# Performance work log

Hardware: AMD Instinct MI355X
Metric: run time of the kernel (lower is better)

Reference implementation:

```python
import jax, jax.numpy as jnp
import numpy as np

N, E, D_IN, HID, HEADS, TS_OUT = 100000, 200000, 165, 64, 8, 5
HD1 = HID // HEADS  # 8 per-head channels in layer 1
HD2 = HID           # 64 per-head channels in layer 2 (concat=False -> mean)


def _glorot(key, shape):
    fan_in, fan_out = shape[0], shape[1]
    s = np.sqrt(6.0 / (fan_in + fan_out)).astype(np.float32)
    return jax.random.uniform(key, shape, jnp.float32, -s, s)


def setup_inputs() -> dict:
    key = jax.random.key(0)
    ks = jax.random.split(key, 24)
    inp = {
        "x": jax.random.normal(ks[0], (N, D_IN), jnp.float32),
        "edge_index": jax.random.randint(ks[1], (2, E), 0, N, jnp.int32),
        "timestamp_target": jax.random.randint(ks[2], (N,), 0, TS_OUT, jnp.int32),
        "node_target": jax.random.randint(ks[3], (N,), 0, 2, jnp.int32),
        "node_mask": jax.random.randint(ks[4], (N,), 0, 2, jnp.int32).astype(jnp.bool_),
        # GATConv layer 1: in=165 -> 8 heads x 8 ch, concat -> 64
        "W1": _glorot(ks[5], (D_IN, HEADS * HD1)),
        "att_src1": _glorot(ks[6], (HEADS, HD1)),
        "att_dst1": _glorot(ks[7], (HEADS, HD1)),
        "b1": jnp.zeros((HEADS * HD1,), jnp.float32),
        # GATConv layer 2: in=64 -> 8 heads x 64 ch, mean -> 64
        "W2": _glorot(ks[8], (HID, HEADS * HD2)),
        "att_src2": _glorot(ks[9], (HEADS, HD2)),
        "att_dst2": _glorot(ks[10], (HEADS, HD2)),
        "b2": jnp.zeros((HD2,), jnp.float32),
        # timestamp predictor MLP
        "ts_w1": _glorot(ks[11], (HID, HID)), "ts_b1": jnp.zeros((HID,), jnp.float32),
        "ts_w2": _glorot(ks[12], (HID, TS_OUT)), "ts_b2": jnp.zeros((TS_OUT,), jnp.float32),
        # class predictor MLP
        "cls_w1": _glorot(ks[13], (HID, HID)), "cls_b1": jnp.zeros((HID,), jnp.float32),
        "cls_w2": _glorot(ks[14], (HID, 2)), "cls_b2": jnp.zeros((2,), jnp.float32),
    }
    return inp


def _gat_layer(x, src, dst, n, W, a_src, a_dst, b, concat):
    H, C = a_src.shape
    h = (x @ W).reshape(n, H, C)                      # [N,H,C]
    a_s = (h * a_src).sum(-1)                         # [N,H]
    a_d = (h * a_dst).sum(-1)                         # [N,H]
    alpha = jax.nn.leaky_relu(a_s[src] + a_d[dst], 0.2)   # [E,H]
    amax = jax.ops.segment_max(alpha, dst, num_segments=n)
    ea = jnp.exp(alpha - amax[dst])
    denom = jax.ops.segment_sum(ea, dst, num_segments=n)
    a = ea / (denom[dst] + 1e-16)                     # segment softmax over incoming edges
    out = jax.ops.segment_sum(h[src] * a[:, :, None], dst, num_segments=n)  # [N,H,C]
    out = out.reshape(n, H * C) if concat else out.mean(axis=1)
    return out + b


def _ce(logits, targets):
    lp = jax.nn.log_softmax(logits, axis=-1)
    return -jnp.take_along_axis(lp, targets[:, None].astype(jnp.int32), axis=1)[:, 0]


def reference(x, edge_index, timestamp_target, node_target, node_mask,
              W1, att_src1, att_dst1, b1, W2, att_src2, att_dst2, b2,
              ts_w1, ts_b1, ts_w2, ts_b2, cls_w1, cls_b1, cls_w2, cls_b2):
    n = x.shape[0]
    loops = jnp.arange(n, dtype=edge_index.dtype)
    src = jnp.concatenate([edge_index[0], loops])     # add self loops (PyG default)
    dst = jnp.concatenate([edge_index[1], loops])
    h = _gat_layer(x, src, dst, n, W1, att_src1, att_dst1, b1, True)   # [N,64]
    h = _gat_layer(h, src, dst, n, W2, att_src2, att_dst2, b2, False)  # [N,64]
    # gradient reversal is identity in the forward pass
    ts_pred = jax.nn.relu(h @ ts_w1 + ts_b1) @ ts_w2 + ts_b2           # [N,5]
    cls_pred = jax.nn.relu(h @ cls_w1 + cls_b1) @ cls_w2 + cls_b2      # [N,2]
    ts_loss = _ce(ts_pred, timestamp_target).mean()
    m = node_mask.astype(jnp.float32)
    cls_loss = (_ce(cls_pred, node_target) * m).sum() / m.sum()
    return cls_loss + 1.0 * ts_loss
```

## Files before the change

### kernel.cpp

```cpp
#include <hip/hip_runtime.h>
#include <hip/hip_bf16.h>

#define NN 100000
#define NE 200000
#define NT (NE + NN)
#define DIN 165
#define PREPB 128
#define INITB 391
#define PACKB 32
#define W1PB 24
#define MISCGRID (PREPB + INITB + PACKB + W1PB)
#define NODEB 1563
#define XDW ((size_t)NN * DIN)
#define G1ROWS 32
#define G1NDMA 21

typedef __attribute__((ext_vector_type(8))) short bf16x8_t;
typedef __attribute__((ext_vector_type(4))) float f32x4_t;
typedef _Float16 h2_t __attribute__((ext_vector_type(2)));
typedef _Float16 f16x8_t __attribute__((ext_vector_type(8)));

#define AS1 __attribute__((address_space(1)))
#define AS3 __attribute__((address_space(3)))

static __device__ __forceinline__ unsigned short f2bf(float f) {
    __hip_bfloat16 b = __float2bfloat16(f);
    return *(unsigned short*)&b;
}
static __device__ __forceinline__ float bfu(unsigned short u) {
    __hip_bfloat16 b = *(__hip_bfloat16*)&u;
    return __bfloat162float(b);
}
static __device__ __forceinline__ unsigned pkh2(float a, float b) {
    h2_t v; v[0] = (_Float16)a; v[1] = (_Float16)b;
    return *(unsigned*)&v;
}


__global__ __launch_bounds__(256) void k_misc(const float* W2, const float* a2s, const float* a2d,
                                              float* wsd, __hip_bfloat16* W2pT,
                                              int* cnt, int* fill,
                                              const float* tsw1, const float* cw1,
                                              __hip_bfloat16* wB,
                                              const float* W1, unsigned* W1pT, float* zbuf) {
    int b = blockIdx.x;
    int tid = threadIdx.x;
    if (b < PREPB) {
        int i = b * 256 + tid;
        int c = i >> 9, j = i & 511;
        int hh = j >> 6, kk = j & 63;
        W2pT[i] = __float2bfloat16(W2[kk * 512 + hh * 64 + c]);
        if (b == 0) zbuf[tid] = 0.f;
        if (i < 512) {
            int h = i >> 6, k = i & 63;
            float s = 0.f, d = 0.f;
            for (int cc = 0; cc < 64; cc++) {
                float w = W2[k * 512 + h * 64 + cc];
                s += w * a2s[h * 64 + cc];
                d += w * a2d[h * 64 + cc];
            }
            wsd[i] = s; wsd[512 + i] = d;
        }
    } else if (b < PREPB + INITB) {
        int i = (b - PREPB) * 256 + tid;
        if (i < NN) { cnt[i] = 0; fill[i] = 0; }
    } else if (b < PREPB + INITB + PACKB) {
        int i = (b - PREPB - INITB) * 256 + tid;
        if (i < 8192) {
            int c = i >> 6, k = i & 63;
            float v = (c < 64) ? tsw1[k * 64 + c] : cw1[k * 64 + (c - 64)];
            wB[i] = __float2bfloat16(v);
        }
    } else {
        int i = (b - PREPB - INITB - PACKB) * 256 + tid;
        if (i < 6144) {
            int c = i / 96, kp = i - c * 96;
            int k = 2 * kp;
            float f0 = (k < DIN) ? W1[k * 64 + c] : 0.f;
            float f1 = (k + 1 < DIN) ? W1[(k + 1) * 64 + c] : 0.f;
            W1pT[i] = pkh2(f0, f1);
        }
    }
}


__global__ __launch_bounds__(256) void k_count(const int* dstE, int* cnt) {
    int e = blockIdx.x * 256 + threadIdx.x;
    if (e < NE) atomicAdd(&cnt[dstE[e]], 1);
}

__global__ __launch_bounds__(256) void k_scanA(const int* cnt, int* rowptr, int* bsum) {
    __shared__ int sm[256];
    int t = threadIdx.x;
    int base = blockIdx.x * 1024;
    int v[4]; int s = 0;
    for (int i = 0; i < 4; i++) {
        int idx = base + t * 4 + i;
        v[i] = (idx < NN) ? (cnt[idx] + 1) : 0;
        s += v[i];
    }
    sm[t] = s; __syncthreads();
    for (int off = 1; off < 256; off <<= 1) {
        int x = (t >= off) ? sm[t - off] : 0;
        __syncthreads();
        sm[t] += x;
        __syncthreads();
    }
    int run = sm[t] - s;
    for (int i = 0; i < 4; i++) {
        run += v[i];
        int idx = base + t * 4 + i;
        if (idx < NN) rowptr[idx + 1] = run;
    }
    if (t == 255) bsum[blockIdx.x] = sm[255];
}

__global__ __launch_bounds__(64) void k_scanB(int* bsum, int nb) {
    int lane = threadIdx.x;
    int v0 = (lane < nb) ? bsum[lane] : 0;
    int v1 = (64 + lane < nb) ? bsum[64 + lane] : 0;
    int s0 = v0;
    for (int off = 1; off < 64; off <<= 1) { int t = __shfl_up(s0, off); if (lane >= off) s0 += t; }
    int tot0 = __shfl(s0, 63);
    int s1 = v1;
    for (int off = 1; off < 64; off <<= 1) { int t = __shfl_up(s1, off); if (lane >= off) s1 += t; }
    if (lane < nb) bsum[lane] = s0 - v0;
    if (64 + lane < nb) bsum[64 + lane] = tot0 + s1 - v1;
}

__global__ __launch_bounds__(256) void k_scanC(const int* bsum, int* rowptr) {
    int i = blockIdx.x * 256 + threadIdx.x;
    if (i < NN) rowptr[i + 1] += bsum[i >> 10];
    if (i == 0) rowptr[0] = 0;
}

__global__ __launch_bounds__(256) void k_fill(const int* srcE, const int* dstE,
                                              const int* rowptr, int* fill, int* col, int* rowv) {
    int i = blockIdx.x * 256 + threadIdx.x;
    if (i >= NT) return;
    int s, d;
    if (i < NE) { s = srcE[i]; d = dstE[i]; }
    else        { s = i - NE; d = s; }
    int p = rowptr[d] + atomicAdd(&fill[d], 1);
    col[p] = s;
    rowv[p] = d;
}


__global__ __launch_bounds__(128) void k_gemm1(const float* x, const unsigned* W1pT,
                                               const float* att_s, const float* att_d,
                                               const float* zsrc,
                                               __hip_bfloat16* h1b, float* aad1) {
    __shared__ float X[G1NDMA * 256];
    int tid = threadIdx.x;
    int l = tid & 63, w = tid >> 6;
    int n0 = blockIdx.x * G1ROWS;
    int frow = l & 15, kg = l >> 4;

    size_t tb = (size_t)n0 * DIN;
    for (int i = w; i < G1NDMA; i += 2) {
        size_t gd = tb + (size_t)i * 256 + (size_t)l * 4;
        const float* g = (gd + 4 <= XDW) ? (x + gd) : (zsrc + l * 4);
        __builtin_amdgcn_global_load_lds((const AS1 float*)g,
                                         (AS3 float*)(X + i * 256), 16, 0, 0);
    }
    uint4 B[6][4];
    #pragma unroll
    for (int s = 0; s < 6; s++)
        #pragma unroll
        for (int t = 0; t < 4; t++)
            B[s][t] = *(const uint4*)&W1pT[(t * 16 + frow) * 96 + s * 16 + kg * 4];
    __syncthreads();

    f32x4_t acc[4] = {};
    int rbase = (w * 16 + frow) * DIN + kg * 8;
    #pragma unroll
    for (int s = 0; s < 6; s++) {
        f16x8_t av;
        #pragma unroll
        for (int j = 0; j < 8; j++) av[j] = (_Float16)X[rbase + s * 32 + j];
        #pragma unroll
        for (int t = 0; t < 4; t++)
            acc[t] = __builtin_amdgcn_mfma_f32_16x16x32_f16(av, *(f16x8_t*)&B[s][t], acc[t], 0, 0, 0);
    }

    int nw = n0 + w * 16;
    float asv[4], adv[4];
    #pragma unroll
    for (int t = 0; t < 4; t++) {
        int c = t * 16 + frow;
        asv[t] = att_s[c]; adv[t] = att_d[c];
    }
    int hb = (l >> 3) & 1;
    #pragma unroll
    for (int q = 0; q < 4; q++) {
        int n = nw + kg * 4 + q;
        #pragma unroll
        for (int t = 0; t < 4; t++) {
            float sv = acc[t][q] * asv[t];
            float dv = acc[t][q] * adv[t];
            sv += __shfl_xor(sv, 1); sv += __shfl_xor(sv, 2); sv += __shfl_xor(sv, 4);
            dv += __shfl_xor(dv, 1); dv += __shfl_xor(dv, 2); dv += __shfl_xor(dv, 4);
            if ((l & 7) == 0) {
                int h = t * 2 + hb;
                aad1[(size_t)n * 16 + h]     = sv;
                aad1[(size_t)n * 16 + 8 + h] = dv;
            }
        }
    }

    __syncthreads();
    unsigned short* Hw = (unsigned short*)X + w * 1152;
    #pragma unroll
    for (int t = 0; t < 4; t++)
        #pragma unroll
        for (int q = 0; q < 4; q++)
            Hw[(kg * 4 + q) * 72 + t * 16 + frow] = f2bf(acc[t][q]);
    int rr = l >> 2, cc = l & 3;
    int n2 = nw + rr;
    unsigned short* dst = (unsigned short*)h1b + (size_t)n2 * 64 + cc * 16;
    *(uint4*)dst       = *(const uint4*)&Hw[rr * 72 + cc * 16];
    *(uint4*)(dst + 8) = *(const uint4*)&Hw[rr * 72 + cc * 16 + 8];
}


__global__ __launch_bounds__(256) void k_edgew(const float* aad, const int* col, const int* rowv,
                                               __hip_bfloat16* web) {
    int e = blockIdx.x * 256 + threadIdx.x;
    if (e >= NT) return;
    int s = col[e], d = rowv[e];
    float4 s0 = *(const float4*)&aad[(size_t)s * 16];
    float4 s1 = *(const float4*)&aad[(size_t)s * 16 + 4];
    float4 dd0 = *(const float4*)&aad[(size_t)d * 16 + 8];
    float4 dd1 = *(const float4*)&aad[(size_t)d * 16 + 12];
    float as[8] = {s0.x, s0.y, s0.z, s0.w, s1.x, s1.y, s1.z, s1.w};
    float ad[8] = {dd0.x, dd0.y, dd0.z, dd0.w, dd1.x, dd1.y, dd1.z, dd1.w};
    unsigned p[4];
    #pragma unroll
    for (int q = 0; q < 4; q++) {
        float a0 = as[2*q]   + ad[2*q];
        float a1 = as[2*q+1] + ad[2*q+1];
        a0 = a0 > 0.f ? a0 : 0.2f * a0;
        a1 = a1 > 0.f ? a1 : 0.2f * a1;
        p[q] = (unsigned)f2bf(__expf(a0)) | ((unsigned)f2bf(__expf(a1)) << 16);
    }
    *(uint4*)&web[(size_t)e * 8] = make_uint4(p[0], p[1], p[2], p[3]);
}


__global__ __launch_bounds__(256) void k_agg1(const __hip_bfloat16* h1b, const __hip_bfloat16* we1b,
                                              const int* rowptr, const int* col,
                                              const float* b1, __hip_bfloat16* out1b) {
    int tid = threadIdx.x;
    int q = tid & 15;
    int n = blockIdx.x * 16 + (tid >> 4);
    int hq = q >> 1;
    const unsigned short* h1u = (const unsigned short*)h1b;
    const unsigned short* weu = (const unsigned short*)we1b;
    int rs = rowptr[n], re = rowptr[n + 1];
    float acc0 = 0.f, acc1 = 0.f, acc2 = 0.f, acc3 = 0.f, den = 0.f;
    for (int eb = rs; eb < re; eb += 4) {
        int c4[4];
        #pragma unroll
        for (int j = 0; j < 4; j++) c4[j] = col[min(eb + j, re - 1)];
        #pragma unroll
        for (int j = 0; j < 4; j++) {
            int e = min(eb + j, re - 1);
            float wv = bfu(weu[(size_t)e * 8 + hq]);
            wv = (eb + j < re) ? wv : 0.f;
            uint2 hv = *(const uint2*)&h1u[(size_t)c4[j] * 64 + q * 4];
            den  += wv;
            acc0 += wv * bfu((unsigned short)(hv.x & 0xffff));
            acc1 += wv * bfu((unsigned short)(hv.x >> 16));
            acc2 += wv * bfu((unsigned short)(hv.y & 0xffff));
            acc3 += wv * bfu((unsigned short)(hv.y >> 16));
        }
    }
    float4 bb = *(const float4*)&b1[q * 4];
    float dd = den + 1e-16f;
    unsigned short* ou = (unsigned short*)out1b;
    unsigned p0 = (unsigned)f2bf(acc0 / dd + bb.x) | ((unsigned)f2bf(acc1 / dd + bb.y) << 16);
    unsigned p1 = (unsigned)f2bf(acc2 / dd + bb.z) | ((unsigned)f2bf(acc3 / dd + bb.w) << 16);
    *(uint2*)&ou[(size_t)n * 64 + q * 4] = make_uint2(p0, p1);
}


__global__ __launch_bounds__(256) void k_att2(const __hip_bfloat16* out1b, const float* wsd,
                                              float* aad2) {
    __shared__ float t[64][65];
    int tid = threadIdx.x;
    int n0 = blockIdx.x * 64;
    const unsigned short* o1u = (const unsigned short*)out1b;
    #pragma unroll
    for (int l = 0; l < 4; l++) {
        int q = tid + l * 256;
        int r = q >> 4, c4 = q & 15;
        int n = n0 + r;
        uint2 v = make_uint2(0, 0);
        if (n < NN) v = *(const uint2*)&o1u[(size_t)n * 64 + c4 * 4];
        t[r][c4 * 4 + 0] = bfu((unsigned short)(v.x & 0xffff));
        t[r][c4 * 4 + 1] = bfu((unsigned short)(v.x >> 16));
        t[r][c4 * 4 + 2] = bfu((unsigned short)(v.y & 0xffff));
        t[r][c4 * 4 + 3] = bfu((unsigned short)(v.y >> 16));
    }
    __syncthreads();
    int lane = tid & 63;
    int j0 = __builtin_amdgcn_readfirstlane((tid >> 6) * 4);
    int n = n0 + lane;
    float a0 = 0.f, a1 = 0.f, a2 = 0.f, a3 = 0.f;
    #pragma unroll 8
    for (int k = 0; k < 64; k++) {
        float ov = t[lane][k];
        a0 += ov * wsd[(j0 + 0) * 64 + k];
        a1 += ov * wsd[(j0 + 1) * 64 + k];
        a2 += ov * wsd[(j0 + 2) * 64 + k];
        a3 += ov * wsd[(j0 + 3) * 64 + k];
    }
    if (n < NN) *(float4*)&aad2[(size_t)n * 16 + j0] = make_float4(a0, a1, a2, a3);
}


__global__ __launch_bounds__(256) void k_l2f(const __hip_bfloat16* out1b, const __hip_bfloat16* we2b,
                                             const int* rowptr, const int* col,
                                             const __hip_bfloat16* W2pT, const float* b2,
                                             const __hip_bfloat16* wB,
                                             const float* tsb1, const float* cb1,
                                             const float* tsw2, const float* tsb2,
                                             const float* cw2, const float* cb2,
                                             const int* tst, const int* ctg, const unsigned char* msk,
                                             float* part) {
    __shared__ unsigned short Ax[64 * 512];
    __shared__ unsigned short Bl[64 * 72];
    __shared__ float red[4][3];
    int tid = threadIdx.x;
    int l = tid & 63, w = tid >> 6;
    int n0 = blockIdx.x * 64;
    int frow = l & 15, kg = l >> 4;

    const unsigned short* o1u = (const unsigned short*)out1b;
    const unsigned short* weu = (const unsigned short*)we2b;
    int q4 = tid & 15;
    #pragma unroll 1
    for (int pass = 0; pass < 4; pass++) {
        int j = pass * 16 + (tid >> 4);
        int n = n0 + j;
        int rs = 0, re = 0;
        if (n < NN) { rs = rowptr[n]; re = rowptr[n + 1]; }
        float acc[8][4];
        float den[8];
        #pragma unroll
        for (int h = 0; h < 8; h++) {
            den[h] = 0.f;
            #pragma unroll
            for (int c = 0; c < 4; c++) acc[h][c] = 0.f;
        }
        for (int eb = rs; eb < re; eb += 4) {
            int c4[4];
            #pragma unroll
            for (int jj = 0; jj < 4; jj++) c4[jj] = col[min(eb + jj, re - 1)];
            #pragma unroll
            for (int jj = 0; jj < 4; jj++) {
                int e = min(eb + jj, re - 1);
                uint4 wv = *(const uint4*)&weu[(size_t)e * 8];
                uint2 hv = *(const uint2*)&o1u[(size_t)c4[jj] * 64 + q4 * 4];
                float vm = (eb + jj < re) ? 1.f : 0.f;
                float hc0 = bfu((unsigned short)(hv.x & 0xffff));
                float hc1 = bfu((unsigned short)(hv.x >> 16));
                float hc2 = bfu((unsigned short)(hv.y & 0xffff));
                float hc3 = bfu((unsigned short)(hv.y >> 16));
                float wt[8] = {bfu((unsigned short)(wv.x & 0xffff)), bfu((unsigned short)(wv.x >> 16)),
                               bfu((unsigned short)(wv.y & 0xffff)), bfu((unsigned short)(wv.y >> 16)),
                               bfu((unsigned short)(wv.z & 0xffff)), bfu((unsigned short)(wv.z >> 16)),
                               bfu((unsigned short)(wv.w & 0xffff)), bfu((unsigned short)(wv.w >> 16))};
                #pragma unroll
                for (int h = 0; h < 8; h++) {
                    float ww = wt[h] * vm;
                    den[h] += ww;
                    acc[h][0] += ww * hc0;
                    acc[h][1] += ww * hc1;
                    acc[h][2] += ww * hc2;
                    acc[h][3] += ww * hc3;
                }
            }
        }
        #pragma unroll
        for (int h = 0; h < 8; h++) {
            float dd = den[h] + 1e-16f;
            unsigned lo = (unsigned)f2bf(acc[h][0] / dd) | ((unsigned)f2bf(acc[h][1] / dd) << 16);
            unsigned hi = (unsigned)f2bf(acc[h][2] / dd) | ((unsigned)f2bf(acc[h][3] / dd) << 16);
            int blk = (h * 8 + (q4 >> 1)) ^ (j & 7);
            *(uint2*)&Ax[j * 512 + blk * 8 + (q4 & 1) * 4] = make_uint2(lo, hi);
        }
    }
    __syncthreads();

    const unsigned short* B_g = (const unsigned short*)W2pT;
    f32x4_t gacc[4] = {};
    for (int k0 = 0; k0 < 512; k0 += 64) {
        #pragma unroll
        for (int ll = 0; ll < 2; ll++) {
            int u = tid + ll * 256;
            int r = u >> 3, seg = u & 7;
            *(uint4*)&Bl[r * 72 + seg * 8] = *(const uint4*)&B_g[(size_t)r * 512 + k0 + seg * 8];
        }
        __syncthreads();
        #pragma unroll
        for (int kk = 0; kk < 2; kk++) {
            int blk = ((k0 >> 3) + kk * 4 + kg) ^ (frow & 7);
            bf16x8_t a = *(const bf16x8_t*)&Ax[(w * 16 + frow) * 512 + blk * 8];
            #pragma unroll
            for (int t = 0; t < 4; t++) {
                bf16x8_t bb = *(const bf16x8_t*)&Bl[(t * 16 + frow) * 72 + kk * 32 + kg * 8];
                gacc[t] = __builtin_amdgcn_mfma_f32_16x16x32_bf16(a, bb, gacc[t], 0, 0, 0);
            }
        }
        __syncthreads();
    }

    unsigned short* o2L = Ax;
    #pragma unroll
    for (int t = 0; t < 4; t++) {
        float bias = b2[t * 16 + frow];
        #pragma unroll
        for (int q = 0; q < 4; q++)
            o2L[(w * 16 + kg * 4 + q) * 72 + t * 16 + frow] = f2bf(0.125f * gacc[t][q] + bias);
    }
    __syncthreads();
    const unsigned short* wBu = (const unsigned short*)wB;
    f32x4_t a2c[8] = {};
    #pragma unroll
    for (int kk = 0; kk < 2; kk++) {
        bf16x8_t a2 = *(const bf16x8_t*)&o2L[(w * 16 + frow) * 72 + kk * 32 + kg * 8];
        #pragma unroll
        for (int t2 = 0; t2 < 8; t2++) {
            bf16x8_t b2f = *(const bf16x8_t*)&wBu[(t2 * 16 + frow) * 64 + kk * 32 + kg * 8];
            a2c[t2] = __builtin_amdgcn_mfma_f32_16x16x32_bf16(a2, b2f, a2c[t2], 0, 0, 0);
        }
    }

    float lg[4][5]; float lc[4][2];
    #pragma unroll
    for (int q = 0; q < 4; q++) {
        #pragma unroll
        for (int t = 0; t < 5; t++) lg[q][t] = 0.f;
        lc[q][0] = 0.f; lc[q][1] = 0.f;
    }
    #pragma unroll
    for (int t2 = 0; t2 < 4; t2++) {
        int c = t2 * 16 + frow;
        float bb = tsb1[c];
        float w0 = tsw2[c * 5 + 0], w1 = tsw2[c * 5 + 1], w2 = tsw2[c * 5 + 2],
              w3 = tsw2[c * 5 + 3], w4 = tsw2[c * 5 + 4];
        #pragma unroll
        for (int q = 0; q < 4; q++) {
            float v = fmaxf(a2c[t2][q] + bb, 0.f);
            lg[q][0] += v * w0; lg[q][1] += v * w1; lg[q][2] += v * w2;
            lg[q][3] += v * w3; lg[q][4] += v * w4;
        }
    }
    #pragma unroll
    for (int t2 = 0; t2 < 4; t2++) {
        int c = t2 * 16 + frow;
        float bb = cb1[c];
        float u0 = cw2[c * 2], u1 = cw2[c * 2 + 1];
        #pragma unroll
        for (int q = 0; q < 4; q++) {
            float v = fmaxf(a2c[t2 + 4][q] + bb, 0.f);
            lc[q][0] += v * u0; lc[q][1] += v * u1;
        }
    }
    #pragma unroll
    for (int q = 0; q < 4; q++) {
        #pragma unroll
        for (int t = 0; t < 5; t++) {
            lg[q][t] += __shfl_xor(lg[q][t], 1);
            lg[q][t] += __shfl_xor(lg[q][t], 2);
            lg[q][t] += __shfl_xor(lg[q][t], 4);
            lg[q][t] += __shfl_xor(lg[q][t], 8);
        }
        #pragma unroll
        for (int t = 0; t < 2; t++) {
            lc[q][t] += __shfl_xor(lc[q][t], 1);
            lc[q][t] += __shfl_xor(lc[q][t], 2);
            lc[q][t] += __shfl_xor(lc[q][t], 4);
            lc[q][t] += __shfl_xor(lc[q][t], 8);
        }
    }
    float tsl = 0.f, cll = 0.f, mval = 0.f;
    if (frow == 0) {
        #pragma unroll
        for (int q = 0; q < 4; q++) {
            int n = n0 + w * 16 + kg * 4 + q;
            if (n < NN) {
                float L[5];
                #pragma unroll
                for (int t = 0; t < 5; t++) L[t] = lg[q][t] + tsb2[t];
                float mx = fmaxf(fmaxf(fmaxf(L[0], L[1]), fmaxf(L[2], L[3])), L[4]);
                float se = 0.f;
                #pragma unroll
                for (int t = 0; t < 5; t++) se += __expf(L[t] - mx);
                int tg = tst[n];
                float pick = 0.f;
                #pragma unroll
                for (int t = 0; t < 5; t++) pick += (t == tg) ? L[t] : 0.f;
                tsl += mx + __logf(se) - pick;
                float C0 = lc[q][0] + cb2[0];
                float C1 = lc[q][1] + cb2[1];
                float mx2 = fmaxf(C0, C1);
                float lse2 = mx2 + __logf(__expf(C0 - mx2) + __expf(C1 - mx2));
                float mv = msk[n] ? 1.f : 0.f;
                float pick2 = ctg[n] ? C1 : C0;
                cll += (lse2 - pick2) * mv;
                mval += mv;
            }
        }
    }
    #pragma unroll
    for (int off = 1; off < 64; off <<= 1) {
        tsl  += __shfl_xor(tsl, off);
        cll  += __shfl_xor(cll, off);
        mval += __shfl_xor(mval, off);
    }
    if (l == 0) { red[w][0] = tsl; red[w][1] = cll; red[w][2] = mval; }
    __syncthreads();
    if (tid == 0) {
        part[blockIdx.x * 3 + 0] = red[0][0] + red[1][0] + red[2][0] + red[3][0];
        part[blockIdx.x * 3 + 1] = red[0][1] + red[1][1] + red[2][1] + red[3][1];
        part[blockIdx.x * 3 + 2] = red[0][2] + red[1][2] + red[2][2] + red[3][2];
    }
}

__global__ __launch_bounds__(256) void k_final(const float* part, float* out, int nb) {
    __shared__ float sm[3][256];
    int tid = threadIdx.x;
    float a = 0, b = 0, c = 0;
    for (int i = tid; i < nb; i += 256) { a += part[i*3]; b += part[i*3+1]; c += part[i*3+2]; }
    sm[0][tid] = a; sm[1][tid] = b; sm[2][tid] = c;
    __syncthreads();
    for (int s = 128; s > 0; s >>= 1) {
        if (tid < s) {
            sm[0][tid] += sm[0][tid + s];
            sm[1][tid] += sm[1][tid + s];
            sm[2][tid] += sm[2][tid + s];
        }
        __syncthreads();
    }
    if (tid == 0) out[0] = sm[1][0] / sm[2][0] + sm[0][0] / (float)NN;
}


extern "C" void kernel_launch(void* const* d_in, const int* in_sizes, int n_in,
                              void* d_out, int out_size, void* d_ws, size_t ws_size,
                              hipStream_t stream) {
    const float* x    = (const float*)d_in[0];
    const int*   ei   = (const int*)d_in[1];
    const int*   tst  = (const int*)d_in[2];
    const int*   ctg  = (const int*)d_in[3];
    const unsigned char* msk = (const unsigned char*)d_in[4];
    const float* W1   = (const float*)d_in[5];
    const float* a1s  = (const float*)d_in[6];
    const float* a1d  = (const float*)d_in[7];
    const float* b1   = (const float*)d_in[8];
    const float* W2   = (const float*)d_in[9];
    const float* a2s  = (const float*)d_in[10];
    const float* a2d  = (const float*)d_in[11];
    const float* b2   = (const float*)d_in[12];
    const float* tsw1 = (const float*)d_in[13];
    const float* tsb1 = (const float*)d_in[14];
    const float* tsw2 = (const float*)d_in[15];
    const float* tsb2 = (const float*)d_in[16];
    const float* cw1  = (const float*)d_in[17];
    const float* cb1  = (const float*)d_in[18];
    const float* cw2  = (const float*)d_in[19];
    const float* cb2  = (const float*)d_in[20];
    const int* srcE = ei;
    const int* dstE = ei + NE;

    char* ws = (char*)d_ws;
    size_t off = 0;
    auto alloc = [&](size_t b) { size_t o = off; off = (off + b + 255) & ~(size_t)255; return o; };
    int*   cnt    = (int*)(ws + alloc((size_t)NN * 4));
    int*   fill   = (int*)(ws + alloc((size_t)NN * 4));
    int*   rowptr = (int*)(ws + alloc((size_t)(NN + 1) * 4));
    int*   bsum   = (int*)(ws + alloc(128 * 4));
    int*   col    = (int*)(ws + alloc((size_t)NT * 4));
    int*   rowv   = (int*)(ws + alloc((size_t)NT * 4));
    float* aad1   = (float*)(ws + alloc((size_t)NN * 16 * 4));
    __hip_bfloat16* out1b = (__hip_bfloat16*)(ws + alloc((size_t)NN * 64 * 2));
    float* aad2   = (float*)(ws + alloc((size_t)NN * 16 * 4));
    float* wsd    = (float*)(ws + alloc(1024 * 4));
    __hip_bfloat16* W2pT  = (__hip_bfloat16*)(ws + alloc(32768 * 2));
    __hip_bfloat16* wB    = (__hip_bfloat16*)(ws + alloc(8192 * 2));
    unsigned* W1pT = (unsigned*)(ws + alloc(6144 * 4));
    float* zbuf   = (float*)(ws + alloc(256 * 4));
    __hip_bfloat16* h1b   = (__hip_bfloat16*)(ws + alloc((size_t)NN * 64 * 2));
    __hip_bfloat16* web   = (__hip_bfloat16*)(ws + alloc((size_t)NT * 8 * 2));
    float* part   = (float*)(ws + alloc((size_t)NODEB * 3 * 4));
    (void)ws_size; (void)in_sizes; (void)n_in; (void)out_size;

    int nb_scan = (NN + 1023) / 1024;

    k_misc<<<MISCGRID, 256, 0, stream>>>(W2, a2s, a2d, wsd, W2pT, cnt, fill,
                                         tsw1, cw1, wB, W1, W1pT, zbuf);
    k_count<<<(NE + 255) / 256, 256, 0, stream>>>(dstE, cnt);
    k_scanA<<<nb_scan, 256, 0, stream>>>(cnt, rowptr, bsum);
    k_scanB<<<1, 64, 0, stream>>>(bsum, nb_scan);
    k_scanC<<<(NN + 255) / 256, 256, 0, stream>>>(bsum, rowptr);
    k_fill<<<(NT + 255) / 256, 256, 0, stream>>>(srcE, dstE, rowptr, fill, col, rowv);

    k_gemm1<<<NN / G1ROWS, 128, 0, stream>>>(x, W1pT, a1s, a1d, zbuf, h1b, aad1);
    k_edgew<<<(NT + 255) / 256, 256, 0, stream>>>(aad1, col, rowv, web);
    k_agg1<<<NN / 16, 256, 0, stream>>>(h1b, web, rowptr, col, b1, out1b);
    k_att2<<<NODEB, 256, 0, stream>>>(out1b, wsd, aad2);
    k_edgew<<<(NT + 255) / 256, 256, 0, stream>>>(aad2, col, rowv, web);

    k_l2f<<<NODEB, 256, 0, stream>>>(out1b, web, rowptr, col, W2pT, b2, wB,
                                     tsb1, cb1, tsw2, tsb2, cw2, cb2, tst, ctg, msk, part);

    k_final<<<1, 256, 0, stream>>>(part, (float*)d_out, NODEB);
}
```

Before: 196.2 us.

## Halve k_l2f block rows, stream W2 from registers, split MLP heads across waves

The fused layer-2/MLP kernel now handles 32 nodes per block instead of 64. That halves the LDS footprint and doubles the grid, which should raise occupancy and parallelism for the gather phase. The W2 GEMM drops its LDS staging of B and the per-step barriers. Each wave instead double-buffers its B fragments directly from global memory into registers, and waves split by row and column tiles. The MLP heads are split across wave pairs (ts vs cls), and bounds checks are removed on the assumption that N divides 32, at the cost of redundant global reads of W2 per wave.

```diff
diff --git a/kernel.cpp b/kernel.cpp
--- a/kernel.cpp
+++ b/kernel.cpp
@@ -14,6 +14,7 @@
 #define XDW ((size_t)NN * DIN)
 #define G1ROWS 32
 #define G1NDMA 21
+#define L2ROWS 32
 
 typedef __attribute__((ext_vector_type(8))) short bf16x8_t;
 typedef __attribute__((ext_vector_type(4))) float f32x4_t;
@@ -329,23 +330,21 @@
                                              const float* cw2, const float* cb2,
                                              const int* tst, const int* ctg, const unsigned char* msk,
                                              float* part) {
-    __shared__ unsigned short Ax[64 * 512];
-    __shared__ unsigned short Bl[64 * 72];
+    __shared__ unsigned short Ax[L2ROWS * 512];
     __shared__ float red[4][3];
     int tid = threadIdx.x;
     int l = tid & 63, w = tid >> 6;
-    int n0 = blockIdx.x * 64;
+    int n0 = blockIdx.x * L2ROWS;
     int frow = l & 15, kg = l >> 4;
 
     const unsigned short* o1u = (const unsigned short*)out1b;
     const unsigned short* weu = (const unsigned short*)we2b;
     int q4 = tid & 15;
     #pragma unroll 1
-    for (int pass = 0; pass < 4; pass++) {
+    for (int pass = 0; pass < 2; pass++) {
         int j = pass * 16 + (tid >> 4);
         int n = n0 + j;
-        int rs = 0, re = 0;
-        if (n < NN) { rs = rowptr[n]; re = rowptr[n + 1]; }
+        int rs = rowptr[n], re = rowptr[n + 1];
         float acc[8][4];
         float den[8];
         #pragma unroll
@@ -394,104 +393,96 @@
     }
     __syncthreads();
 
-    const unsigned short* B_g = (const unsigned short*)W2pT;
-    f32x4_t gacc[4] = {};
+    const unsigned short* Bg = (const unsigned short*)W2pT;
+    int r0 = (w & 1) * 16;
+    int c0 = (w >> 1) * 32;
+    f32x4_t gacc[2] = {};
+    uint4 rBa00, rBa01, rBa10, rBa11;
+    rBa00 = *(const uint4*)&Bg[(size_t)(c0 + frow) * 512 + 0 * 32 + kg * 8];
+    rBa01 = *(const uint4*)&Bg[(size_t)(c0 + frow) * 512 + 1 * 32 + kg * 8];
+    rBa10 = *(const uint4*)&Bg[(size_t)(c0 + 16 + frow) * 512 + 0 * 32 + kg * 8];
+    rBa11 = *(const uint4*)&Bg[(size_t)(c0 + 16 + frow) * 512 + 1 * 32 + kg * 8];
+    #pragma unroll
     for (int k0 = 0; k0 < 512; k0 += 64) {
-        #pragma unroll
-        for (int ll = 0; ll < 2; ll++) {
-            int u = tid + ll * 256;
-            int r = u >> 3, seg = u & 7;
-            *(uint4*)&Bl[r * 72 + seg * 8] = *(const uint4*)&B_g[(size_t)r * 512 + k0 + seg * 8];
-        }
-        __syncthreads();
+        uint4 rBb00, rBb01, rBb10, rBb11;
+        if (k0 < 448) {
+            int kn = k0 + 64;
+            rBb00 = *(const uint4*)&Bg[(size_t)(c0 + frow) * 512 + kn + 0 * 32 + kg * 8];
+            rBb01 = *(const uint4*)&Bg[(size_t)(c0 + frow) * 512 + kn + 1 * 32 + kg * 8];
+            rBb10 = *(const uint4*)&Bg[(size_t)(c0 + 16 + frow) * 512 + kn + 0 * 32 + kg * 8];
+            rBb11 = *(const uint4*)&Bg[(size_t)(c0 + 16 + frow) * 512 + kn + 1 * 32 + kg * 8];
+        }
         #pragma unroll
         for (int kk = 0; kk < 2; kk++) {
-            int blk = ((k0 >> 3) + kk * 4 + kg) ^ (frow & 7);
-            bf16x8_t a = *(const bf16x8_t*)&Ax[(w * 16 + frow) * 512 + blk * 8];
-            #pragma unroll
-            for (int t = 0; t < 4; t++) {
-                bf16x8_t bb = *(const bf16x8_t*)&Bl[(t * 16 + frow) * 72 + kk * 32 + kg * 8];
-                gacc[t] = __builtin_amdgcn_mfma_f32_16x16x32_bf16(a, bb, gacc[t], 0, 0, 0);
-            }
-        }
-        __syncthreads();
-    }
+            int bidx = (k0 >> 3) + kk * 4 + kg;
+            int blk = bidx ^ (frow & 7);
+            bf16x8_t a = *(const bf16x8_t*)&Ax[(r0 + frow) * 512 + blk * 8];
+            gacc[0] = __builtin_amdgcn_mfma_f32_16x16x32_bf16(
+                a, *(bf16x8_t*)(kk == 0 ? &rBa00 : &rBa01), gacc[0], 0, 0, 0);
+            gacc[1] = __builtin_amdgcn_mfma_f32_16x16x32_bf16(
+                a, *(bf16x8_t*)(kk == 0 ? &rBa10 : &rBa11), gacc[1], 0, 0, 0);
+        }
+        rBa00 = rBb00; rBa01 = rBb01; rBa10 = rBb10; rBa11 = rBb11;
+    }
+    __syncthreads();
 
     unsigned short* o2L = Ax;
     #pragma unroll
-    for (int t = 0; t < 4; t++) {
-        float bias = b2[t * 16 + frow];
+    for (int t = 0; t < 2; t++) {
+        float bias = b2[c0 + t * 16 + frow];
+        f32x4_t g = gacc[t];
         #pragma unroll
         for (int q = 0; q < 4; q++)
-            o2L[(w * 16 + kg * 4 + q) * 72 + t * 16 + frow] = f2bf(0.125f * gacc[t][q] + bias);
+            o2L[(r0 + kg * 4 + q) * 72 + c0 + t * 16 + frow] = f2bf(0.125f * g[q] + bias);
     }
     __syncthreads();
     const unsigned short* wBu = (const unsigned short*)wB;
-    f32x4_t a2c[8] = {};
+    int m0 = (w & 1) * 16;
+    int h0 = (w >> 1) * 64;
+    f32x4_t a2c[4] = {};
     #pragma unroll
     for (int kk = 0; kk < 2; kk++) {
-        bf16x8_t a2 = *(const bf16x8_t*)&o2L[(w * 16 + frow) * 72 + kk * 32 + kg * 8];
-        #pragma unroll
-        for (int t2 = 0; t2 < 8; t2++) {
-            bf16x8_t b2f = *(const bf16x8_t*)&wBu[(t2 * 16 + frow) * 64 + kk * 32 + kg * 8];
-            a2c[t2] = __builtin_amdgcn_mfma_f32_16x16x32_bf16(a2, b2f, a2c[t2], 0, 0, 0);
-        }
-    }
-
-    float lg[4][5]; float lc[4][2];
-    #pragma unroll
-    for (int q = 0; q < 4; q++) {
-        #pragma unroll
-        for (int t = 0; t < 5; t++) lg[q][t] = 0.f;
-        lc[q][0] = 0.f; lc[q][1] = 0.f;
-    }
-    #pragma unroll
-    for (int t2 = 0; t2 < 4; t2++) {
-        int c = t2 * 16 + frow;
-        float bb = tsb1[c];
-        float w0 = tsw2[c * 5 + 0], w1 = tsw2[c * 5 + 1], w2 = tsw2[c * 5 + 2],
-              w3 = tsw2[c * 5 + 3], w4 = tsw2[c * 5 + 4];
-        #pragma unroll
-        for (int q = 0; q < 4; q++) {
-            float v = fmaxf(a2c[t2][q] + bb, 0.f);
-            lg[q][0] += v * w0; lg[q][1] += v * w1; lg[q][2] += v * w2;
-            lg[q][3] += v * w3; lg[q][4] += v * w4;
-        }
-    }
-    #pragma unroll
-    for (int t2 = 0; t2 < 4; t2++) {
-        int c = t2 * 16 + frow;
-        float bb = cb1[c];
-        float u0 = cw2[c * 2], u1 = cw2[c * 2 + 1];
-        #pragma unroll
-        for (int q = 0; q < 4; q++) {
-            float v = fmaxf(a2c[t2 + 4][q] + bb, 0.f);
-            lc[q][0] += v * u0; lc[q][1] += v * u1;
-        }
-    }
-    #pragma unroll
-    for (int q = 0; q < 4; q++) {
-        #pragma unroll
-        for (int t = 0; t < 5; t++) {
-            lg[q][t] += __shfl_xor(lg[q][t], 1);
-            lg[q][t] += __shfl_xor(lg[q][t], 2);
-            lg[q][t] += __shfl_xor(lg[q][t], 4);
-            lg[q][t] += __shfl_xor(lg[q][t], 8);
-        }
-        #pragma unroll
-        for (int t = 0; t < 2; t++) {
-            lc[q][t] += __shfl_xor(lc[q][t], 1);
-            lc[q][t] += __shfl_xor(lc[q][t], 2);
-            lc[q][t] += __shfl_xor(lc[q][t], 4);
-            lc[q][t] += __shfl_xor(lc[q][t], 8);
-        }
-    }
+        bf16x8_t a2 = *(const bf16x8_t*)&o2L[(m0 + frow) * 72 + kk * 32 + kg * 8];
+        #pragma unroll
+        for (int t2 = 0; t2 < 4; t2++) {
+            bf16x8_t bf = *(const bf16x8_t*)&wBu[(h0 + t2 * 16 + frow) * 64 + kk * 32 + kg * 8];
+            a2c[t2] = __builtin_amdgcn_mfma_f32_16x16x32_bf16(a2, bf, a2c[t2], 0, 0, 0);
+        }
+    }
+
     float tsl = 0.f, cll = 0.f, mval = 0.f;
-    if (frow == 0) {
-        #pragma unroll
-        for (int q = 0; q < 4; q++) {
-            int n = n0 + w * 16 + kg * 4 + q;
-            if (n < NN) {
+    if ((w >> 1) == 0) {
+        float lg[4][5];
+        #pragma unroll
+        for (int q = 0; q < 4; q++)
+            #pragma unroll
+            for (int t = 0; t < 5; t++) lg[q][t] = 0.f;
+        #pragma unroll
+        for (int t2 = 0; t2 < 4; t2++) {
+            int c = t2 * 16 + frow;
+            float bb = tsb1[c];
+            float w0 = tsw2[c * 5 + 0], w1 = tsw2[c * 5 + 1], w2 = tsw2[c * 5 + 2],
+                  w3 = tsw2[c * 5 + 3], w4 = tsw2[c * 5 + 4];
+            #pragma unroll
+            for (int q = 0; q < 4; q++) {
+                float v = fmaxf(a2c[t2][q] + bb, 0.f);
+                lg[q][0] += v * w0; lg[q][1] += v * w1; lg[q][2] += v * w2;
+                lg[q][3] += v * w3; lg[q][4] += v * w4;
+            }
+        }
+        #pragma unroll
+        for (int q = 0; q < 4; q++)
+            #pragma unroll
+            for (int t = 0; t < 5; t++) {
+                lg[q][t] += __shfl_xor(lg[q][t], 1);
+                lg[q][t] += __shfl_xor(lg[q][t], 2);
+                lg[q][t] += __shfl_xor(lg[q][t], 4);
+                lg[q][t] += __shfl_xor(lg[q][t], 8);
+            }
+        if (frow == 0) {
+            #pragma unroll
+            for (int q = 0; q < 4; q++) {
+                int n = n0 + m0 + kg * 4 + q;
                 float L[5];
                 #pragma unroll
                 for (int t = 0; t < 5; t++) L[t] = lg[q][t] + tsb2[t];
@@ -504,6 +495,36 @@
                 #pragma unroll
                 for (int t = 0; t < 5; t++) pick += (t == tg) ? L[t] : 0.f;
                 tsl += mx + __logf(se) - pick;
+            }
+        }
+    } else {
+        float lc[4][2];
+        #pragma unroll
+        for (int q = 0; q < 4; q++) { lc[q][0] = 0.f; lc[q][1] = 0.f; }
+        #pragma unroll
+        for (int t2 = 0; t2 < 4; t2++) {
+            int c = t2 * 16 + frow;
+            float bb = cb1[c];
+            float u0 = cw2[c * 2], u1 = cw2[c * 2 + 1];
+            #pragma unroll
+            for (int q = 0; q < 4; q++) {
+                float v = fmaxf(a2c[t2][q] + bb, 0.f);
+                lc[q][0] += v * u0; lc[q][1] += v * u1;
+            }
+        }
+        #pragma unroll
+        for (int q = 0; q < 4; q++)
+            #pragma unroll
+            for (int t = 0; t < 2; t++) {
+                lc[q][t] += __shfl_xor(lc[q][t], 1);
+                lc[q][t] += __shfl_xor(lc[q][t], 2);
+                lc[q][t] += __shfl_xor(lc[q][t], 4);
+                lc[q][t] += __shfl_xor(lc[q][t], 8);
+            }
+        if (frow == 0) {
+            #pragma unroll
+            for (int q = 0; q < 4; q++) {
+                int n = n0 + m0 + kg * 4 + q;
                 float C0 = lc[q][0] + cb2[0];
                 float C1 = lc[q][1] + cb2[1];
                 float mx2 = fmaxf(C0, C1);
@@ -595,7 +616,7 @@
     float* zbuf   = (float*)(ws + alloc(256 * 4));
     __hip_bfloat16* h1b   = (__hip_bfloat16*)(ws + alloc((size_t)NN * 64 * 2));
     __hip_bfloat16* web   = (__hip_bfloat16*)(ws + alloc((size_t)NT * 8 * 2));
-    float* part   = (float*)(ws + alloc((size_t)NODEB * 3 * 4));
+    float* part   = (float*)(ws + alloc((size_t)(NN / L2ROWS) * 3 * 4));
     (void)ws_size; (void)in_sizes; (void)n_in; (void)out_size;
 
     int nb_scan = (NN + 1023) / 1024;
@@ -614,8 +635,8 @@
     k_att2<<<NODEB, 256, 0, stream>>>(out1b, wsd, aad2);
     k_edgew<<<(NT + 255) / 256, 256, 0, stream>>>(aad2, col, rowv, web);
 
-    k_l2f<<<NODEB, 256, 0, stream>>>(out1b, web, rowptr, col, W2pT, b2, wB,
-                                     tsb1, cb1, tsw2, tsb2, cw2, cb2, tst, ctg, msk, part);
-
-    k_final<<<1, 256, 0, stream>>>(part, (float*)d_out, NODEB);
-}
+    k_l2f<<<NN / L2ROWS, 256, 0, stream>>>(out1b, web, rowptr, col, W2pT, b2, wB,
+                                           tsb1, cb1, tsw2, tsb2, cw2, cb2, tst, ctg, msk, part);
+
+    k_final<<<1, 256, 0, stream>>>(part, (float*)d_out, NN / L2ROWS);
+}
```

Result: no change. 199.7 us (+1.8%).
